# Kernel tuning notes

Hardware: AMD Instinct MI355X
Metric: run time of the kernel (lower is better)

Reference implementation:

```python
import jax, jax.numpy as jnp
import numpy as np

S = 8      # max segment id present in masks
D = 768    # hidden size (hardcoded in the torch module)
N_VIS = 100  # leading vision tokens in vision_trace_feat


def _segment_mean(feat, mask, n_seg):
    """Per-(batch, seg_id) mean of feat tokens where mask == seg_id.
    feat: [B, L, D], mask: [B, L] ints in 0..n_seg. Returns means [B, n_seg, D], counts [B, n_seg].
    Equivalent to the torch loop over seg_id + split + per-chunk mean(dim=0)."""
    onehot = (mask[:, :, None] == jnp.arange(1, n_seg + 1)[None, None, :]).astype(feat.dtype)  # [B,L,S]
    sums = jnp.einsum('bls,bld->bsd', onehot, feat)   # [B,S,D]
    counts = onehot.sum(axis=1)                        # [B,S]
    means = sums / jnp.maximum(counts, 1.0)[:, :, None]
    return means, counts


def setup_inputs() -> dict:
    key = jax.random.key(0)
    k1, k2, k3, k4, k5, k6 = jax.random.split(key, 6)
    B = 64
    vision_trace_feat = jax.random.normal(k1, (B, N_VIS + 412, D), dtype=jnp.float32)
    vision_trace_mask = jnp.sort(jax.random.randint(k2, (B, 412), 0, S + 1), axis=-1).astype(jnp.int32)
    caption_feat = jax.random.normal(k3, (B, 512, D), dtype=jnp.float32)
    caption_mask = jnp.sort(jax.random.randint(k4, (B, 513), 0, S + 1), axis=-1).astype(jnp.int32)
    vt_merge_w = jax.random.normal(k5, (2 * D, D), dtype=jnp.float32) * 0.02
    vt_merge_b = jax.random.normal(k6, (D,), dtype=jnp.float32) * 0.02
    return {
        'vision_trace_feat': vision_trace_feat,
        'vision_trace_mask': vision_trace_mask,
        'caption_feat': caption_feat,
        'caption_mask': caption_mask,
        'vt_merge_w': vt_merge_w,
        'vt_merge_b': vt_merge_b,
    }


def reference(vision_trace_feat, vision_trace_mask, caption_feat, caption_mask, vt_merge_w, vt_merge_b):
    # --- CaptionAggregator (meanpool) ---
    cm = caption_mask[:, 1:]                                   # drop CLS position
    c_means, c_counts = _segment_mean(caption_feat, cm, S)      # [B,S,D], [B,S]
    c_present = (c_counts > 0).astype(c_means.dtype)
    caption_out = c_means * c_present[:, :, None]               # dense form: empty segments zeroed

    # --- VisionTraceAggregator (meanpool) ---
    vision_feat = vision_trace_feat[:, :N_VIS].mean(axis=1)     # [B,D]
    trace_feat = vision_trace_feat[:, N_VIS:]                   # [B,Lt,D]
    t_means, t_counts = _segment_mean(trace_feat, vision_trace_mask, S)
    t_present = (t_counts > 0).astype(t_means.dtype)
    vt = jnp.concatenate(
        [t_means, jnp.broadcast_to(vision_feat[:, None, :], t_means.shape)], axis=-1)  # [B,S,2D]
    vt_out = (vt @ vt_merge_w + vt_merge_b) * t_present[:, :, None]
    return (caption_out, vt_out)
```

## Files before the change

### kernel.cpp

```cpp
#include <hip/hip_runtime.h>
#include <hip/hip_bf16.h>

#define SEGS   8
#define DIM    768
#define NVIS   100
#define BATCH  64
#define LTOK   512
#define NCHK   8
#define TPC    64
#define KS     8
#define KLEN   96

#define OFF_PCAP  0
#define OFF_PTRC  (OFF_PCAP + BATCH*NCHK*SEGS*DIM)
#define OFF_PVIS  (OFF_PTRC + BATCH*NCHK*SEGS*DIM)
#define OFF_PCCNT (OFF_PVIS + BATCH*2*DIM)
#define OFF_PTCNT (OFF_PCCNT + BATCH*NCHK*SEGS)
#define OFF_TMEAN (OFF_PTCNT + BATCH*NCHK*SEGS)
#define OFF_TCNT  (OFF_TMEAN + BATCH*9*DIM)
#define OFF_PGEM  0


__global__ __launch_bounds__(192) void reduce_kernel(
    const float* __restrict__ vt_feat,
    const int* __restrict__ vt_mask,
    const float* __restrict__ cap_feat,
    const int* __restrict__ cap_mask,
    float* __restrict__ ws)
{
    const int bid  = blockIdx.x;
    const int type = bid >> 10;
    const int b    = (bid >> 4) & 63;
    const int ck   = (bid >> 1) & 7;
    const int half = bid & 1;
    const int tid  = threadIdx.x;
    const int c0   = half * 384 + tid * 2;

    __shared__ __align__(16) int msk[TPC];
    __shared__ int scnt[SEGS + 1];
    if (tid < SEGS + 1) scnt[tid] = 0;
    if (tid < TPC) {
        const int l = ck * TPC + tid;
        int m;
        if (type == 0) m = cap_mask[b * 513 + 1 + l];
        else           m = (l >= NVIS) ? vt_mask[b * 412 + (l - NVIS)] : 0;
        msk[tid] = m;
    }
    __syncthreads();
    if (half == 0 && tid < TPC) {
        const int m = msk[tid]; if (m > 0) atomicAdd(&scnt[m], 1);
    }

    float acc[SEGS][2];
#pragma unroll
    for (int s = 0; s < SEGS; ++s) { acc[s][0] = 0.f; acc[s][1] = 0.f; }
    float vacc[2] = {0.f, 0.f};
    float tmp[2]  = {0.f, 0.f};
    int cur = 0;

    const float* __restrict__ feat = (type == 0) ? cap_feat : vt_feat;
    const size_t base = (size_t)b * LTOK * DIM + (size_t)c0;

    for (int j = 0; j < TPC; j += 8) {
        const float* p = feat + base + (size_t)(ck * TPC + j) * DIM;
        float2 v[8];
#pragma unroll
        for (int u = 0; u < 8; ++u)
            v[u] = *reinterpret_cast<const float2*>(p + (size_t)u * DIM);
        const int4 m4a = *reinterpret_cast<const int4*>(&msk[j]);
        const int4 m4b = *reinterpret_cast<const int4*>(&msk[j + 4]);
        const int mm[8] = {m4a.x, m4a.y, m4a.z, m4a.w,
                           m4b.x, m4b.y, m4b.z, m4b.w};
#pragma unroll
        for (int u = 0; u < 8; ++u) {
            const int l = ck * TPC + j + u;
            if (type == 1 && l < NVIS) {
                vacc[0] += v[u].x; vacc[1] += v[u].y;
            } else {
                const int m = __builtin_amdgcn_readfirstlane(mm[u]);
                if (m != cur) {
#pragma unroll
                    for (int s = 0; s < SEGS; ++s)
                        if (cur == s + 1) {
                            acc[s][0] += tmp[0]; acc[s][1] += tmp[1];
                        }
                    tmp[0] = 0.f; tmp[1] = 0.f;
                    cur = m;
                }
                tmp[0] += v[u].x; tmp[1] += v[u].y;
            }
        }
    }
#pragma unroll
    for (int s = 0; s < SEGS; ++s)
        if (cur == s + 1) {
            acc[s][0] += tmp[0]; acc[s][1] += tmp[1];
        }

    __syncthreads();

    float* __restrict__ pbase = ws + (type == 0 ? OFF_PCAP : OFF_PTRC)
                              + ((size_t)(b * NCHK + ck) * SEGS) * DIM + c0;
#pragma unroll
    for (int s = 0; s < SEGS; ++s) {
        *reinterpret_cast<float2*>(pbase + s * DIM) =
            make_float2(acc[s][0], acc[s][1]);
    }
    if (half == 0) {
        int* __restrict__ cbase = (int*)(ws + (type == 0 ? OFF_PCCNT : OFF_PTCNT))
                                + (b * NCHK + ck) * SEGS;
        if (tid < SEGS) cbase[tid] = scnt[tid + 1];
    }
    if (type == 1 && ck < 2) {
        *reinterpret_cast<float2*>(ws + OFF_PVIS + (size_t)(b * 2 + ck) * DIM + c0) =
            make_float2(vacc[0], vacc[1]);
    }
}

__global__ __launch_bounds__(256) void combine1_kernel(
    const float* __restrict__ ws_c, float* __restrict__ ws,
    float* __restrict__ out)
{
    const int i = blockIdx.x * 256 + threadIdx.x;
    const int CAPN = BATCH * SEGS * DIM;
    if (i < CAPN) {
        const int b = i / (SEGS * DIM);
        const int r = i % (SEGS * DIM);
        const int s = r / DIM, d = r % DIM;
        float sum = 0.f; int c = 0;
#pragma unroll
        for (int ck = 0; ck < NCHK; ++ck) {
            sum += ws_c[OFF_PCAP + ((size_t)((b * NCHK + ck) * SEGS + s)) * DIM + d];
            c   += ((const int*)(ws_c + OFF_PCCNT))[(b * NCHK + ck) * SEGS + s];
        }
        out[i] = (c > 0) ? sum / (float)c : 0.f;
    } else if (i < 2 * CAPN) {
        const int j = i - CAPN;
        const int b = j / (SEGS * DIM);
        const int r = j % (SEGS * DIM);
        const int s = r / DIM, d = r % DIM;
        float sum = 0.f; int c = 0;
#pragma unroll
        for (int ck = 0; ck < NCHK; ++ck) {
            sum += ws_c[OFF_PTRC + ((size_t)((b * NCHK + ck) * SEGS + s)) * DIM + d];
            c   += ((const int*)(ws_c + OFF_PTCNT))[(b * NCHK + ck) * SEGS + s];
        }
        ws[OFF_TMEAN + ((size_t)(b * 9 + s)) * DIM + d] = (c > 0) ? sum / (float)c : 0.f;
        if (d == 0) ((int*)(ws + OFF_TCNT))[b * SEGS + s] = c;
    } else {
        const int j = i - 2 * CAPN;
        const int b = j / DIM, d = j % DIM;
        ws[OFF_TMEAN + ((size_t)(b * 9 + 8)) * DIM + d] =
            (ws_c[OFF_PVIS + (size_t)(b * 2 + 0) * DIM + d] +
             ws_c[OFF_PVIS + (size_t)(b * 2 + 1) * DIM + d]) * (1.0f / (float)NVIS);
    }
}

__global__ __launch_bounds__(192) void gemm_kernel(
    const float* __restrict__ W,
    const float* __restrict__ ws_c,
    float* __restrict__ ws)
{
    const int b   = blockIdx.x >> 3;
    const int kc  = blockIdx.x & 7;
    const int k0  = kc * KLEN;
    const int tid = threadIdx.x;

    __shared__ __align__(16) float As[9][KLEN];
    for (int i = tid; i < 9 * KLEN; i += 192) {
        const int r = i / KLEN, k = i % KLEN;
        As[r][k] = ws_c[OFF_TMEAN + ((size_t)(b * 9 + r)) * DIM + k0 + k];
    }
    __syncthreads();

    float acc[9][4];
#pragma unroll
    for (int r = 0; r < 9; ++r) { acc[r][0]=0.f; acc[r][1]=0.f; acc[r][2]=0.f; acc[r][3]=0.f; }

    const float* __restrict__ Wt = W + (size_t)k0 * DIM + tid * 4;
    const float* __restrict__ Wb = W + (size_t)(DIM + k0) * DIM + tid * 4;

    for (int k = 0; k < KLEN; k += 4) {
        float a[9][4];
#pragma unroll
        for (int r = 0; r < 9; ++r) {
            const float4 t = *reinterpret_cast<const float4*>(&As[r][k]);
            a[r][0] = t.x; a[r][1] = t.y; a[r][2] = t.z; a[r][3] = t.w;
        }
#pragma unroll
        for (int u = 0; u < 4; ++u) {
            const float4 wt4 = *reinterpret_cast<const float4*>(Wt + (size_t)(k + u) * DIM);
            const float4 wb4 = *reinterpret_cast<const float4*>(Wb + (size_t)(k + u) * DIM);
            const float wt[4] = {wt4.x, wt4.y, wt4.z, wt4.w};
            const float wb[4] = {wb4.x, wb4.y, wb4.z, wb4.w};
#pragma unroll
            for (int r = 0; r < SEGS; ++r) {
#pragma unroll
                for (int j = 0; j < 4; ++j) acc[r][j] += a[r][u] * wt[j];
            }
#pragma unroll
            for (int j = 0; j < 4; ++j) acc[8][j] += a[8][u] * wb[j];
        }
    }

    float* __restrict__ P = ws + OFF_PGEM + ((size_t)(kc * BATCH + b) * 9) * DIM;
#pragma unroll
    for (int r = 0; r < 9; ++r)
        reinterpret_cast<float4*>(P + r * DIM)[tid] =
            make_float4(acc[r][0], acc[r][1], acc[r][2], acc[r][3]);
}

__global__ __launch_bounds__(256) void combine2_kernel(
    const float* __restrict__ bias,
    const float* __restrict__ ws_c,
    float* __restrict__ out)
{
    const int j = blockIdx.x * 256 + threadIdx.x;
    const int HALF = BATCH * SEGS * DIM;
    const int b = j / (SEGS * DIM);
    const int r = j % (SEGS * DIM);
    const int s = r / DIM, d = r % DIM;
    const int c = ((const int*)(ws_c + OFF_TCNT))[b * SEGS + s];
    float v = 0.f;
    if (c > 0) {
        float sum = bias[d];
#pragma unroll
        for (int kc = 0; kc < KS; ++kc) {
            const float* P = ws_c + OFF_PGEM + ((size_t)(kc * BATCH + b) * 9) * DIM;
            sum += P[s * DIM + d] + P[8 * DIM + d];
        }
        v = sum;
    }
    out[HALF + j] = v;
}

extern "C" void kernel_launch(void* const* d_in, const int* in_sizes, int n_in,
                              void* d_out, int out_size, void* d_ws, size_t ws_size,
                              hipStream_t stream) {
    const float* vt_feat  = (const float*)d_in[0];
    const int*   vt_mask  = (const int*)d_in[1];
    const float* cap_feat = (const float*)d_in[2];
    const int*   cap_mask = (const int*)d_in[3];
    const float* W        = (const float*)d_in[4];
    const float* bias     = (const float*)d_in[5];
    float* out = (float*)d_out;
    float* ws = (float*)d_ws;

    reduce_kernel  <<<2048, 192, 0, stream>>>(vt_feat, vt_mask, cap_feat, cap_mask, ws);
    combine1_kernel<<<3264, 256, 0, stream>>>(ws, ws, out);
    gemm_kernel    <<<512, 192, 0, stream>>>(W, ws, ws);
    combine2_kernel<<<1536, 256, 0, stream>>>(bias, ws, out);
}
```

Measured before the change: 283.9 us.

## Fuse trace combine, GEMM and epilogue into one kernel with caption combine

Replaces the combine1, split-K GEMM and combine2 kernels with a single kernel. 64 blocks each reduce one batch's trace partials into shared memory and run the full K=768 GEMM with bias and mask epilogue. The remaining blocks do the caption mean combine. This removes two launches and the workspace round trips for means and GEMM partials, but the GEMM now runs on only 64 blocks with a long serial K loop, so there is much less parallelism per batch.

```diff
diff --git a/kernel.cpp b/kernel.cpp
--- a/kernel.cpp
+++ b/kernel.cpp
@@ -8,17 +8,12 @@
 #define LTOK   512
 #define NCHK   8
 #define TPC    64
-#define KS     8
-#define KLEN   96
 
 #define OFF_PCAP  0
 #define OFF_PTRC  (OFF_PCAP + BATCH*NCHK*SEGS*DIM)
 #define OFF_PVIS  (OFF_PTRC + BATCH*NCHK*SEGS*DIM)
 #define OFF_PCCNT (OFF_PVIS + BATCH*2*DIM)
 #define OFF_PTCNT (OFF_PCCNT + BATCH*NCHK*SEGS)
-#define OFF_TMEAN (OFF_PTCNT + BATCH*NCHK*SEGS)
-#define OFF_TCNT  (OFF_TMEAN + BATCH*9*DIM)
-#define OFF_PGEM  0
 
 
 __global__ __launch_bounds__(192) void reduce_kernel(
@@ -117,13 +112,89 @@
     }
 }
 
-__global__ __launch_bounds__(256) void combine1_kernel(
-    const float* __restrict__ ws_c, float* __restrict__ ws,
+__global__ __launch_bounds__(256) void fused_kernel(
+    const float* __restrict__ W,
+    const float* __restrict__ bias,
+    const float* __restrict__ ws_c,
     float* __restrict__ out)
 {
-    const int i = blockIdx.x * 256 + threadIdx.x;
-    const int CAPN = BATCH * SEGS * DIM;
-    if (i < CAPN) {
+    const int bid = blockIdx.x;
+    const int tid = threadIdx.x;
+    const int HALF = BATCH * SEGS * DIM;
+
+    __shared__ __align__(16) float tmean[9][DIM];
+    __shared__ int scnt[SEGS];
+
+    if (bid < BATCH) {
+        const int b = bid;
+        if (tid < SEGS) {
+            int c = 0;
+#pragma unroll
+            for (int ck = 0; ck < NCHK; ++ck)
+                c += ((const int*)(ws_c + OFF_PTCNT))[(b * NCHK + ck) * SEGS + tid];
+            scnt[tid] = c;
+        }
+        __syncthreads();
+
+        for (int idx = tid; idx < SEGS * DIM; idx += 256) {
+            const int s = idx / DIM, k = idx % DIM;
+            float sum = 0.f;
+#pragma unroll
+            for (int ck = 0; ck < NCHK; ++ck)
+                sum += ws_c[OFF_PTRC + ((size_t)((b * NCHK + ck) * SEGS + s)) * DIM + k];
+            const int c = scnt[s];
+            tmean[s][k] = (c > 0) ? sum / (float)c : 0.f;
+        }
+        for (int k = tid; k < DIM; k += 256) {
+            tmean[8][k] = (ws_c[OFF_PVIS + (size_t)(b * 2 + 0) * DIM + k] +
+                           ws_c[OFF_PVIS + (size_t)(b * 2 + 1) * DIM + k]) * (1.0f / (float)NVIS);
+        }
+        __syncthreads();
+
+        if (tid < 192) {
+            const int d0 = tid * 4;
+            float acc[9][4];
+#pragma unroll
+            for (int r = 0; r < 9; ++r) { acc[r][0]=0.f; acc[r][1]=0.f; acc[r][2]=0.f; acc[r][3]=0.f; }
+
+            for (int k = 0; k < DIM; k += 4) {
+                float a[9][4];
+#pragma unroll
+                for (int r = 0; r < 9; ++r) {
+                    const float4 t = *reinterpret_cast<const float4*>(&tmean[r][k]);
+                    a[r][0] = t.x; a[r][1] = t.y; a[r][2] = t.z; a[r][3] = t.w;
+                }
+#pragma unroll
+                for (int u = 0; u < 4; ++u) {
+                    const float4 wt4 = *reinterpret_cast<const float4*>(&W[(size_t)(k + u) * DIM + d0]);
+                    const float4 wb4 = *reinterpret_cast<const float4*>(&W[(size_t)(DIM + k + u) * DIM + d0]);
+                    const float wt[4] = {wt4.x, wt4.y, wt4.z, wt4.w};
+                    const float wb[4] = {wb4.x, wb4.y, wb4.z, wb4.w};
+#pragma unroll
+                    for (int r = 0; r < SEGS; ++r) {
+#pragma unroll
+                        for (int j = 0; j < 4; ++j) acc[r][j] += a[r][u] * wt[j];
+                    }
+#pragma unroll
+                    for (int j = 0; j < 4; ++j) acc[8][j] += a[8][u] * wb[j];
+                }
+            }
+
+            const float4 b4 = *reinterpret_cast<const float4*>(bias + d0);
+            float* __restrict__ o = out + HALF + ((size_t)b * SEGS) * DIM + d0;
+#pragma unroll
+            for (int s = 0; s < SEGS; ++s) {
+                float4 v = make_float4(0.f, 0.f, 0.f, 0.f);
+                if (scnt[s] > 0)
+                    v = make_float4(acc[s][0] + acc[8][0] + b4.x,
+                                    acc[s][1] + acc[8][1] + b4.y,
+                                    acc[s][2] + acc[8][2] + b4.z,
+                                    acc[s][3] + acc[8][3] + b4.w);
+                *reinterpret_cast<float4*>(o + s * DIM) = v;
+            }
+        }
+    } else {
+        const int i = (bid - BATCH) * 256 + tid;
         const int b = i / (SEGS * DIM);
         const int r = i % (SEGS * DIM);
         const int s = r / DIM, d = r % DIM;
@@ -134,104 +205,7 @@
             c   += ((const int*)(ws_c + OFF_PCCNT))[(b * NCHK + ck) * SEGS + s];
         }
         out[i] = (c > 0) ? sum / (float)c : 0.f;
-    } else if (i < 2 * CAPN) {
-        const int j = i - CAPN;
-        const int b = j / (SEGS * DIM);
-        const int r = j % (SEGS * DIM);
-        const int s = r / DIM, d = r % DIM;
-        float sum = 0.f; int c = 0;
-#pragma unroll
-        for (int ck = 0; ck < NCHK; ++ck) {
-            sum += ws_c[OFF_PTRC + ((size_t)((b * NCHK + ck) * SEGS + s)) * DIM + d];
-            c   += ((const int*)(ws_c + OFF_PTCNT))[(b * NCHK + ck) * SEGS + s];
-        }
-        ws[OFF_TMEAN + ((size_t)(b * 9 + s)) * DIM + d] = (c > 0) ? sum / (float)c : 0.f;
-        if (d == 0) ((int*)(ws + OFF_TCNT))[b * SEGS + s] = c;
-    } else {
-        const int j = i - 2 * CAPN;
-        const int b = j / DIM, d = j % DIM;
-        ws[OFF_TMEAN + ((size_t)(b * 9 + 8)) * DIM + d] =
-            (ws_c[OFF_PVIS + (size_t)(b * 2 + 0) * DIM + d] +
-             ws_c[OFF_PVIS + (size_t)(b * 2 + 1) * DIM + d]) * (1.0f / (float)NVIS);
-    }
-}
-
-__global__ __launch_bounds__(192) void gemm_kernel(
-    const float* __restrict__ W,
-    const float* __restrict__ ws_c,
-    float* __restrict__ ws)
-{
-    const int b   = blockIdx.x >> 3;
-    const int kc  = blockIdx.x & 7;
-    const int k0  = kc * KLEN;
-    const int tid = threadIdx.x;
-
-    __shared__ __align__(16) float As[9][KLEN];
-    for (int i = tid; i < 9 * KLEN; i += 192) {
-        const int r = i / KLEN, k = i % KLEN;
-        As[r][k] = ws_c[OFF_TMEAN + ((size_t)(b * 9 + r)) * DIM + k0 + k];
-    }
-    __syncthreads();
-
-    float acc[9][4];
-#pragma unroll
-    for (int r = 0; r < 9; ++r) { acc[r][0]=0.f; acc[r][1]=0.f; acc[r][2]=0.f; acc[r][3]=0.f; }
-
-    const float* __restrict__ Wt = W + (size_t)k0 * DIM + tid * 4;
-    const float* __restrict__ Wb = W + (size_t)(DIM + k0) * DIM + tid * 4;
-
-    for (int k = 0; k < KLEN; k += 4) {
-        float a[9][4];
-#pragma unroll
-        for (int r = 0; r < 9; ++r) {
-            const float4 t = *reinterpret_cast<const float4*>(&As[r][k]);
-            a[r][0] = t.x; a[r][1] = t.y; a[r][2] = t.z; a[r][3] = t.w;
-        }
-#pragma unroll
-        for (int u = 0; u < 4; ++u) {
-            const float4 wt4 = *reinterpret_cast<const float4*>(Wt + (size_t)(k + u) * DIM);
-            const float4 wb4 = *reinterpret_cast<const float4*>(Wb + (size_t)(k + u) * DIM);
-            const float wt[4] = {wt4.x, wt4.y, wt4.z, wt4.w};
-            const float wb[4] = {wb4.x, wb4.y, wb4.z, wb4.w};
-#pragma unroll
-            for (int r = 0; r < SEGS; ++r) {
-#pragma unroll
-                for (int j = 0; j < 4; ++j) acc[r][j] += a[r][u] * wt[j];
-            }
-#pragma unroll
-            for (int j = 0; j < 4; ++j) acc[8][j] += a[8][u] * wb[j];
-        }
-    }
-
-    float* __restrict__ P = ws + OFF_PGEM + ((size_t)(kc * BATCH + b) * 9) * DIM;
-#pragma unroll
-    for (int r = 0; r < 9; ++r)
-        reinterpret_cast<float4*>(P + r * DIM)[tid] =
-            make_float4(acc[r][0], acc[r][1], acc[r][2], acc[r][3]);
-}
-
-__global__ __launch_bounds__(256) void combine2_kernel(
-    const float* __restrict__ bias,
-    const float* __restrict__ ws_c,
-    float* __restrict__ out)
-{
-    const int j = blockIdx.x * 256 + threadIdx.x;
-    const int HALF = BATCH * SEGS * DIM;
-    const int b = j / (SEGS * DIM);
-    const int r = j % (SEGS * DIM);
-    const int s = r / DIM, d = r % DIM;
-    const int c = ((const int*)(ws_c + OFF_TCNT))[b * SEGS + s];
-    float v = 0.f;
-    if (c > 0) {
-        float sum = bias[d];
-#pragma unroll
-        for (int kc = 0; kc < KS; ++kc) {
-            const float* P = ws_c + OFF_PGEM + ((size_t)(kc * BATCH + b) * 9) * DIM;
-            sum += P[s * DIM + d] + P[8 * DIM + d];
-        }
-        v = sum;
-    }
-    out[HALF + j] = v;
+    }
 }
 
 extern "C" void kernel_launch(void* const* d_in, const int* in_sizes, int n_in,
@@ -246,8 +220,6 @@
     float* out = (float*)d_out;
     float* ws = (float*)d_ws;
 
-    reduce_kernel  <<<2048, 192, 0, stream>>>(vt_feat, vt_mask, cap_feat, cap_mask, ws);
-    combine1_kernel<<<3264, 256, 0, stream>>>(ws, ws, out);
-    gemm_kernel    <<<512, 192, 0, stream>>>(W, ws, ws);
-    combine2_kernel<<<1536, 256, 0, stream>>>(bias, ws, out);
+    reduce_kernel<<<2048, 192, 0, stream>>>(vt_feat, vt_mask, cap_feat, cap_mask, ws);
+    fused_kernel <<<BATCH + 1536, 256, 0, stream>>>(W, bias, ws, out);
 }
```

Result: slower. 490.0 us (+72.6%).
